# Kernel optimization log

Hardware: AMD Instinct MI355X
Metric: run time of the kernel (lower is better)

## Reference

```python
import jax, jax.numpy as jnp
import numpy as np

N_HEADS = 16
N_KV_HEADS = 4
HEAD_DIM = 128
NEG_INF = -1e9


def setup_inputs() -> dict:
    key = jax.random.key(0)
    ks = jax.random.split(key, 6)
    bs, seq, d_model = 2, 2048, 2048
    x = jax.random.normal(ks[0], (bs, seq, d_model), jnp.float32)
    # RoPE table: theta = 10000^{-2i/head_dim}, angle = pos * theta
    inv_freq = 1.0 / (10000.0 ** (jnp.arange(0, HEAD_DIM, 2, dtype=jnp.float32) / HEAD_DIM))
    ang = jnp.arange(seq, dtype=jnp.float32)[:, None] * inv_freq[None, :]  # [seq, head_dim/2]
    freqs_cos = jnp.cos(ang)
    freqs_sin = jnp.sin(ang)
    # causal additive mask
    mask = jnp.where(jnp.tril(jnp.ones((seq, seq), dtype=bool)), 0.0, NEG_INF).astype(jnp.float32)
    s = 1.0 / np.sqrt(d_model)
    wq = jax.random.normal(ks[1], (d_model, N_HEADS * HEAD_DIM), jnp.float32) * s
    wk = jax.random.normal(ks[2], (d_model, N_KV_HEADS * HEAD_DIM), jnp.float32) * s
    wv = jax.random.normal(ks[3], (d_model, N_KV_HEADS * HEAD_DIM), jnp.float32) * s
    wo = jax.random.normal(ks[4], (N_HEADS * HEAD_DIM, d_model), jnp.float32) * s
    return {"x": x, "freqs_cos": freqs_cos, "freqs_sin": freqs_sin, "mask": mask,
            "wq": wq, "wk": wk, "wv": wv, "wo": wo}


def _rope(t, cos, sin):
    # t: [b, h, s, d]; cos/sin: [s, d/2]
    b, h, s, d = t.shape
    tp = t.reshape(b, h, s, d // 2, 2)
    x0, x1 = tp[..., 0], tp[..., 1]
    c = cos[None, None, :, :]
    sn = sin[None, None, :, :]
    o0 = x0 * c - x1 * sn
    o1 = x0 * sn + x1 * c
    return jnp.stack([o0, o1], axis=-1).reshape(b, h, s, d)


def reference(x, freqs_cos, freqs_sin, mask, wq, wk, wv, wo):
    bs, seq, d_model = x.shape
    rep = N_HEADS // N_KV_HEADS
    q = (x @ wq).reshape(bs, seq, N_HEADS, HEAD_DIM).transpose(0, 2, 1, 3)
    k = (x @ wk).reshape(bs, seq, N_KV_HEADS, HEAD_DIM).transpose(0, 2, 1, 3)
    v = (x @ wv).reshape(bs, seq, N_KV_HEADS, HEAD_DIM).transpose(0, 2, 1, 3)
    q = _rope(q, freqs_cos, freqs_sin)
    k = _rope(k, freqs_cos, freqs_sin)
    # GQA: group q heads over kv heads instead of materially repeating kv
    qg = q.reshape(bs, N_KV_HEADS, rep, seq, HEAD_DIM)
    scores = jnp.einsum('bgrsd,bgtd->bgrst', qg, k) / np.sqrt(HEAD_DIM)
    scores = scores + mask[None, None, None, :, :]
    attn = jax.nn.softmax(scores, axis=-1)
    out = jnp.einsum('bgrst,bgtd->bgrsd', attn, v)
    out = out.reshape(bs, N_HEADS, seq, HEAD_DIM).transpose(0, 2, 1, 3).reshape(bs, seq, -1)
    return out @ wo
```

## Files before the change

kernel.cpp:

```cpp
#include <hip/hip_runtime.h>
#include <hip/hip_bf16.h>

#define SEQ 2048
#define DM 2048
#define NH 16
#define NKV 4
#define HD 128

typedef float f32x4 __attribute__((ext_vector_type(4)));
typedef short s16x8 __attribute__((ext_vector_type(8)));
typedef short s16x4 __attribute__((ext_vector_type(4)));

__device__ inline __hip_bfloat16 f2b(float f) { return __float2bfloat16(f); }
__device__ inline float b2f_us(unsigned short u) { return __uint_as_float(((unsigned)u) << 16); }
__device__ inline short f2b_s(float f) {
    __hip_bfloat16 h = __float2bfloat16(f);
    return *(short*)&h;
}

__device__ inline void gl_lds16(const void* g, void* l) {
    __builtin_amdgcn_global_load_lds((const __attribute__((address_space(1))) void*)g,
                                     (__attribute__((address_space(3))) void*)l, 16, 0, 0);
}

__global__ void prep_kernel(const float* __restrict__ x,
                            const float* __restrict__ wq, const float* __restrict__ wk,
                            const float* __restrict__ wv, const float* __restrict__ wo,
                            __hip_bfloat16* __restrict__ xb,
                            __hip_bfloat16* __restrict__ wqkvt,
                            __hip_bfloat16* __restrict__ wot) {
    __shared__ float tile[32][33];
    int bid = blockIdx.x;
    const int t = threadIdx.x;
    if (bid < 8192) {
        int i = (bid * 256 + t) * 4;
        float4 v = *(const float4*)(x + i);
        __hip_bfloat16 o4[4] = {f2b(v.x), f2b(v.y), f2b(v.z), f2b(v.w)};
        *(ushort4*)(xb + i) = *(ushort4*)o4;
        return;
    }
    bid -= 8192;
    const float* in;
    __hip_bfloat16* out;
    int N, bx, by;
    if (bid < 4096) {
        in = wq; out = wqkvt; N = 2048; bx = bid & 63; by = bid >> 6;
    } else if (bid < 5120) {
        bid -= 4096; in = wk; out = wqkvt + (size_t)2048 * 2048; N = 512; bx = bid & 15; by = bid >> 4;
    } else if (bid < 6144) {
        bid -= 5120; in = wv; out = wqkvt + (size_t)2560 * 2048; N = 512; bx = bid & 15; by = bid >> 4;
    } else {
        bid -= 6144; in = wo; out = wot; N = 2048; bx = bid & 63; by = bid >> 6;
    }
    const int K = 2048;
    int n0 = bx * 32, k0 = by * 32;
    int tx = t & 31, ty = t >> 5;
    for (int r = ty; r < 32; r += 8)
        tile[r][tx] = in[(size_t)(k0 + r) * N + n0 + tx];
    __syncthreads();
    for (int r = ty; r < 32; r += 8)
        out[(size_t)(n0 + r) * K + k0 + tx] = f2b(tile[tx][r]);
}

template <int OUT_F32>
__global__ __launch_bounds__(256, 3) void gemm_bt(
    const __hip_bfloat16* __restrict__ A,
    const __hip_bfloat16* __restrict__ Bt,
    void* __restrict__ Cp, int M, int N, int Kd) {
    __shared__ __hip_bfloat16 As[128 * 64];
    __shared__ __hip_bfloat16 Bs[128 * 64];
    const int nx = gridDim.x, ny = gridDim.y;
    const int pid = blockIdx.y * nx + blockIdx.x;
    const int GM = 8;
    const int grp = pid / (GM * nx);
    const int first = grp * GM;
    const int gsz = (ny - first < GM) ? (ny - first) : GM;
    const int mt = first + (pid % gsz);
    const int ntile = (pid % (GM * nx)) / gsz;
    const int m0 = mt * 128, n0 = ntile * 128;

    const int t = threadIdx.x;
    const int wv = t >> 6, lane = t & 63;
    const int wm = (wv >> 1) * 64, wn = (wv & 1) * 64;
    const int lrow = lane & 15, quad = lane >> 4;
    f32x4 acc[4][4];
    f32x4 z4 = {0.f, 0.f, 0.f, 0.f};
    for (int i = 0; i < 4; ++i)
        for (int j = 0; j < 4; ++j) acc[i][j] = z4;

    for (int k0 = 0; k0 < Kd; k0 += 64) {
        __syncthreads();
        for (int i = 0; i < 4; ++i) {
            int flat = i * 256 + t;
            int row = flat >> 3;
            int cb = (flat & 7) ^ (row & 7);
            gl_lds16(A + (size_t)(m0 + row) * Kd + k0 + cb * 8, &As[flat * 8]);
            gl_lds16(Bt + (size_t)(n0 + row) * Kd + k0 + cb * 8, &Bs[flat * 8]);
        }
        __syncthreads();
        for (int kk = 0; kk < 2; ++kk) {
            s16x8 af[4], bf[4];
            for (int i = 0; i < 4; ++i) {
                int ra = wm + i * 16 + lrow;
                int rb = wn + i * 16 + lrow;
                int pba = ((kk * 4 + quad) ^ (ra & 7)) * 8;
                int pbb = ((kk * 4 + quad) ^ (rb & 7)) * 8;
                af[i] = *(const s16x8*)&As[ra * 64 + pba];
                bf[i] = *(const s16x8*)&Bs[rb * 64 + pbb];
            }
            for (int i = 0; i < 4; ++i)
                for (int j = 0; j < 4; ++j)
                    acc[i][j] = __builtin_amdgcn_mfma_f32_16x16x32_bf16(af[i], bf[j],
                                                                        acc[i][j], 0, 0, 0);
        }
    }
    for (int i = 0; i < 4; ++i)
        for (int j = 0; j < 4; ++j)
            for (int r = 0; r < 4; ++r) {
                int m = m0 + wm + i * 16 + quad * 4 + r;
                int n = n0 + wn + j * 16 + lrow;
                if (OUT_F32)
                    ((float*)Cp)[(size_t)m * N + n] = acc[i][j][r];
                else
                    ((__hip_bfloat16*)Cp)[(size_t)m * N + n] = f2b(acc[i][j][r]);
            }
}

#define QSC 0.12751744f
__global__ void rv_kernel(const __hip_bfloat16* __restrict__ qkv,
                          const float* __restrict__ fcos, const float* __restrict__ fsin,
                          __hip_bfloat16* __restrict__ q, __hip_bfloat16* __restrict__ k,
                          __hip_bfloat16* __restrict__ vt) {
    __shared__ __hip_bfloat16 tile[128][136];
    const int t = threadIdx.x;
    if (blockIdx.x < 4096) {
        int tok = blockIdx.x;
        int b = tok >> 11, s = tok & 2047;
        const __hip_bfloat16* row = qkv + (size_t)tok * 3072;
        for (int it = t; it < 320; it += 256) {
            int col = it * 8;
            s16x8 v = *(const s16x8*)(row + col);
            int p0 = (col & 127) >> 1;
            f32x4 c4 = *(const f32x4*)(fcos + s * 64 + p0);
            f32x4 s4 = *(const f32x4*)(fsin + s * 64 + p0);
            float scl = (col < 2048) ? QSC : 1.0f;
            short outv[8];
            for (int p = 0; p < 4; ++p) {
                float x0 = b2f_us((unsigned short)v[2 * p]);
                float x1 = b2f_us((unsigned short)v[2 * p + 1]);
                outv[2 * p] = f2b_s((x0 * c4[p] - x1 * s4[p]) * scl);
                outv[2 * p + 1] = f2b_s((x0 * s4[p] + x1 * c4[p]) * scl);
            }
            int d = col & 127;
            if (col < 2048) {
                int h = col >> 7;
                *(s16x8*)(q + ((size_t)((b * NH + h) * SEQ + s)) * HD + d) = *(s16x8*)outv;
            } else {
                int h = (col - 2048) >> 7;
                *(s16x8*)(k + ((size_t)((b * NKV + h) * SEQ + s)) * HD + d) = *(s16x8*)outv;
            }
        }
        return;
    }
    int r = blockIdx.x - 4096;
    int s0 = (r & 15) * 128;
    int bh = r >> 4;
    int b = bh >> 2, kvh = bh & 3;
    for (int i = 0; i < 8; ++i) {
        int flat = (i * 256 + t) * 8;
        int row = flat >> 7, col = flat & 127;
        *(s16x8*)&tile[row][col] =
            *(const s16x8*)(qkv + (size_t)(b * SEQ + s0 + row) * 3072 + 2560 + kvh * 128 + col);
    }
    __syncthreads();
    for (int i = 0; i < 8; ++i) {
        int dd = i * 16 + (t >> 4);
        int ss = (t & 15) * 8;
        __hip_bfloat16 tmp[8];
        for (int j = 0; j < 8; ++j) tmp[j] = tile[ss + j][dd];
        *(s16x8*)(vt + ((size_t)((b * NKV + kvh) * HD + dd)) * SEQ + s0 + ss) = *(s16x8*)tmp;
    }
}

__global__ __launch_bounds__(512, 4) void attn_kernel(
    const __hip_bfloat16* __restrict__ q, const __hip_bfloat16* __restrict__ k,
    const __hip_bfloat16* __restrict__ vt, __hip_bfloat16* __restrict__ o) {
    __shared__ __hip_bfloat16 Ks[2][64][136];
    __shared__ __hip_bfloat16 Vs[2][128][72];

    const int bh = blockIdx.y;
    const int bx = (bh < 16) ? (int)(gridDim.x - 1 - blockIdx.x) : (int)blockIdx.x;
    const int b = bh >> 4, h = bh & 15;
    const int kvh = h >> 2;
    const int t = threadIdx.x;
    const int w = t >> 6, lane = t & 63;
    const int lrow = lane & 15, quad = lane >> 4;
    const int q0 = bx * 128;
    const int qrow = q0 + w * 16 + lrow;

    const __hip_bfloat16* qp = q + ((size_t)((b * NH + h) * SEQ + qrow)) * HD;
    s16x8 qf[4];
    for (int ks = 0; ks < 4; ++ks) qf[ks] = *(const s16x8*)(qp + ks * 32 + quad * 8);

    float m_i = -1e30f, l_i = 0.f;
    f32x4 accO[8];
    f32x4 z4 = {0.f, 0.f, 0.f, 0.f};
    for (int d = 0; d < 8; ++d) accO[d] = z4;

    const __hip_bfloat16* kbase = k + ((size_t)(b * NKV + kvh) * SEQ) * HD;
    const __hip_bfloat16* vbase = vt + ((size_t)(b * NKV + kvh) * HD) * SEQ;

    s16x8 kr[2], vr[2];
    auto load_tile = [&](int kt) {
        for (int i = 0; i < 2; ++i) {
            int flat = (i * 512 + t) * 8;
            kr[i] = *(const s16x8*)(kbase + (size_t)(kt * 64 + (flat >> 7)) * HD + (flat & 127));
            vr[i] = *(const s16x8*)(vbase + (size_t)(flat >> 6) * SEQ + kt * 64 + (flat & 63));
        }
    };
    auto store_tile = [&](int bsel) {
        for (int i = 0; i < 2; ++i) {
            int flat = (i * 512 + t) * 8;
            *(s16x8*)&Ks[bsel][flat >> 7][flat & 127] = kr[i];
            int row = flat >> 6, k0 = flat & 63;
            int pb = ((k0 >> 5) << 5) | (((k0 >> 2) & 2) << 3) | (((k0 >> 4) & 1) << 2);
            s16x4 lo = {vr[i][0], vr[i][1], vr[i][2], vr[i][3]};
            s16x4 hi = {vr[i][4], vr[i][5], vr[i][6], vr[i][7]};
            *(s16x4*)&Vs[bsel][row][pb] = lo;
            *(s16x4*)&Vs[bsel][row][pb + 8] = hi;
        }
    };

    const int nkt = 2 * bx + 2;
    load_tile(0);
    store_tile(0);

    for (int kt = 0; kt < nkt; ++kt) {
        const int cur = kt & 1;
        bool more = (kt + 1) < nkt;
        __syncthreads();
        if (more) load_tile(kt + 1);
        bool wave_active = (kt * 64 <= q0 + w * 16 + 15);
        bool mtile = (kt >= 2 * bx);

        if (wave_active) {
            float sv[4][4];
            __builtin_amdgcn_s_setprio(1);
            for (int nt = 0; nt < 4; ++nt) {
                f32x4 sacc = z4;
                for (int ks = 0; ks < 4; ++ks) {
                    s16x8 kf = *(const s16x8*)&Ks[cur][nt * 16 + lrow][ks * 32 + quad * 8];
                    sacc = __builtin_amdgcn_mfma_f32_16x16x32_bf16(kf, qf[ks], sacc, 0, 0, 0);
                }
                if (mtile) {
                    for (int r = 0; r < 4; ++r) {
                        int key = kt * 64 + nt * 16 + quad * 4 + r;
                        sv[nt][r] = (key > qrow) ? -1e30f : sacc[r];
                    }
                } else {
                    for (int r = 0; r < 4; ++r) sv[nt][r] = sacc[r];
                }
            }
            __builtin_amdgcn_s_setprio(0);
            float mt2 = fmaxf(fmaxf(fmaxf(sv[0][0], sv[0][1]), fmaxf(sv[0][2], sv[0][3])),
                              fmaxf(fmaxf(sv[1][0], sv[1][1]), fmaxf(sv[1][2], sv[1][3])));
            mt2 = fmaxf(mt2,
                        fmaxf(fmaxf(fmaxf(sv[2][0], sv[2][1]), fmaxf(sv[2][2], sv[2][3])),
                              fmaxf(fmaxf(sv[3][0], sv[3][1]), fmaxf(sv[3][2], sv[3][3]))));
            mt2 = fmaxf(mt2, __shfl_xor(mt2, 16, 64));
            mt2 = fmaxf(mt2, __shfl_xor(mt2, 32, 64));
            if (!__all(mt2 <= m_i + 8.f)) {
                float mn = fmaxf(m_i, mt2);
                float alpha = exp2f(m_i - mn);
                l_i *= alpha;
                for (int d = 0; d < 8; ++d)
                    for (int r = 0; r < 4; ++r) accO[d][r] *= alpha;
                m_i = mn;
            }
            float rs = 0.f;
            s16x8 pf0, pf1;
#pragma unroll
            for (int j = 0; j < 8; ++j) {
                float p0 = exp2f(sv[j >> 2][j & 3] - m_i);
                float p1 = exp2f(sv[2 + (j >> 2)][j & 3] - m_i);
                rs += p0 + p1;
                pf0[j] = f2b_s(p0);
                pf1[j] = f2b_s(p1);
            }
            rs += __shfl_xor(rs, 16, 64);
            rs += __shfl_xor(rs, 32, 64);
            l_i += rs;
            __builtin_amdgcn_s_setprio(1);
            for (int dt = 0; dt < 8; ++dt) {
                s16x8 vf0 = *(const s16x8*)&Vs[cur][dt * 16 + lrow][quad * 8];
                s16x8 vf1 = *(const s16x8*)&Vs[cur][dt * 16 + lrow][32 + quad * 8];
                accO[dt] = __builtin_amdgcn_mfma_f32_16x16x32_bf16(vf0, pf0, accO[dt], 0, 0, 0);
                accO[dt] = __builtin_amdgcn_mfma_f32_16x16x32_bf16(vf1, pf1, accO[dt], 0, 0, 0);
            }
            __builtin_amdgcn_s_setprio(0);
        }

        if (more) store_tile(1 - cur);
    }
    float inv = 1.0f / l_i;
    __hip_bfloat16* op = o + (size_t)(b * SEQ + qrow) * DM + h * HD;
    for (int dt = 0; dt < 8; ++dt) {
        short ov[4];
        for (int r = 0; r < 4; ++r) ov[r] = f2b_s(accO[dt][r] * inv);
        *(s16x4*)(op + dt * 16 + quad * 4) = *(s16x4*)ov;
    }
}

extern "C" void kernel_launch(void* const* d_in, const int* in_sizes, int n_in,
                              void* d_out, int out_size, void* d_ws, size_t ws_size,
                              hipStream_t stream) {
    (void)in_sizes; (void)n_in; (void)out_size; (void)ws_size;
    const float* x  = (const float*)d_in[0];
    const float* fc = (const float*)d_in[1];
    const float* fs = (const float*)d_in[2];
    const float* wq = (const float*)d_in[4];
    const float* wk = (const float*)d_in[5];
    const float* wv = (const float*)d_in[6];
    const float* wo = (const float*)d_in[7];

    __hip_bfloat16* xb    = (__hip_bfloat16*)d_ws;
    __hip_bfloat16* wqkvt = xb + (size_t)8388608;
    __hip_bfloat16* wot   = wqkvt + (size_t)6291456;
    __hip_bfloat16* qkv   = wot + (size_t)4194304;
    __hip_bfloat16* qb    = xb;
    __hip_bfloat16* kb    = wqkvt;
    __hip_bfloat16* vtb   = wqkvt + (size_t)2097152;
    __hip_bfloat16* attno = qkv;

    prep_kernel<<<18432, 256, 0, stream>>>(x, wq, wk, wv, wo, xb, wqkvt, wot);
    gemm_bt<0><<<dim3(24, 32), 256, 0, stream>>>(xb, wqkvt, qkv, 4096, 3072, 2048);
    rv_kernel<<<4224, 256, 0, stream>>>(qkv, fc, fs, qb, kb, vtb);
    attn_kernel<<<dim3(16, 32), 512, 0, stream>>>(qb, kb, vtb, attno);
    gemm_bt<1><<<dim3(16, 32), 256, 0, stream>>>(attno, wot, d_out, 4096, 2048, 2048);
}
```

Measured before the change: 325.7 us.

## Rewrite GEMM with 256x256 tiles and 4-stage async LDS pipeline

Replaces the 128x128 single-buffered bf16 GEMM with a 256x256-tile, 512-thread kernel. It streams K in steps of 32 through a 4-deep ring of LDS buffers using global_load_lds and explicit vmcnt waits, so loads overlap the MFMA work. It also adds s_setprio around the MFMA block. The larger tiles increase data reuse and cut barrier overhead, at the cost of more LDS (128KB) and more registers per block. The grids shrink to 192 and 128 blocks, which may underfill the 256 CUs.

```diff
diff --git a/kernel.cpp b/kernel.cpp
--- a/kernel.cpp
+++ b/kernel.cpp
@@ -63,12 +63,13 @@
 }
 
 template <int OUT_F32>
-__global__ __launch_bounds__(256, 3) void gemm_bt(
+__global__ __launch_bounds__(512, 2) void gemm256(
     const __hip_bfloat16* __restrict__ A,
     const __hip_bfloat16* __restrict__ Bt,
     void* __restrict__ Cp, int M, int N, int Kd) {
-    __shared__ __hip_bfloat16 As[128 * 64];
-    __shared__ __hip_bfloat16 Bs[128 * 64];
+    __shared__ __hip_bfloat16 As[4][8192];
+    __shared__ __hip_bfloat16 Bs[4][8192];
+
     const int nx = gridDim.x, ny = gridDim.y;
     const int pid = blockIdx.y * nx + blockIdx.x;
     const int GM = 8;
@@ -77,52 +78,82 @@
     const int gsz = (ny - first < GM) ? (ny - first) : GM;
     const int mt = first + (pid % gsz);
     const int ntile = (pid % (GM * nx)) / gsz;
-    const int m0 = mt * 128, n0 = ntile * 128;
+    const int m0 = mt * 256, n0 = ntile * 256;
 
     const int t = threadIdx.x;
-    const int wv = t >> 6, lane = t & 63;
-    const int wm = (wv >> 1) * 64, wn = (wv & 1) * 64;
+    const int wid = t >> 6, lane = t & 63;
+    const int wr = wid >> 2, wc = wid & 3;
     const int lrow = lane & 15, quad = lane >> 4;
-    f32x4 acc[4][4];
+
+    f32x4 acc[8][4];
     f32x4 z4 = {0.f, 0.f, 0.f, 0.f};
-    for (int i = 0; i < 4; ++i)
+#pragma unroll
+    for (int i = 0; i < 8; ++i)
+#pragma unroll
         for (int j = 0; j < 4; ++j) acc[i][j] = z4;
 
-    for (int k0 = 0; k0 < Kd; k0 += 64) {
-        __syncthreads();
-        for (int i = 0; i < 4; ++i) {
-            int flat = i * 256 + t;
-            int row = flat >> 3;
-            int cb = (flat & 7) ^ (row & 7);
-            gl_lds16(A + (size_t)(m0 + row) * Kd + k0 + cb * 8, &As[flat * 8]);
-            gl_lds16(Bt + (size_t)(n0 + row) * Kd + k0 + cb * 8, &Bs[flat * 8]);
-        }
-        __syncthreads();
-        for (int kk = 0; kk < 2; ++kk) {
-            s16x8 af[4], bf[4];
-            for (int i = 0; i < 4; ++i) {
-                int ra = wm + i * 16 + lrow;
-                int rb = wn + i * 16 + lrow;
-                int pba = ((kk * 4 + quad) ^ (ra & 7)) * 8;
-                int pbb = ((kk * 4 + quad) ^ (rb & 7)) * 8;
-                af[i] = *(const s16x8*)&As[ra * 64 + pba];
-                bf[i] = *(const s16x8*)&Bs[rb * 64 + pbb];
-            }
-            for (int i = 0; i < 4; ++i)
-                for (int j = 0; j < 4; ++j)
-                    acc[i][j] = __builtin_amdgcn_mfma_f32_16x16x32_bf16(af[i], bf[j],
-                                                                        acc[i][j], 0, 0, 0);
-        }
-    }
-    for (int i = 0; i < 4; ++i)
-        for (int j = 0; j < 4; ++j)
+    auto stage = [&](int kt) {
+        const int buf = kt & 3;
+#pragma unroll
+        for (int i = 0; i < 2; ++i) {
+            int slot = i * 512 + t;
+            int row = slot >> 2, p = slot & 3;
+            int cb = p ^ ((row >> 1) & 3);
+            gl_lds16(A + (size_t)(m0 + row) * Kd + kt * 32 + cb * 8, &As[buf][slot * 8]);
+            gl_lds16(Bt + (size_t)(n0 + row) * Kd + kt * 32 + cb * 8, &Bs[buf][slot * 8]);
+        }
+    };
+
+    const int nt = Kd >> 5;
+    stage(0); stage(1); stage(2);
+
+    const int psw = quad ^ ((lrow >> 1) & 3);
+
+    for (int kt = 0; kt < nt; ++kt) {
+        if (kt < nt - 2)
+            asm volatile("s_waitcnt vmcnt(8)" ::: "memory");
+        else if (kt == nt - 2)
+            asm volatile("s_waitcnt vmcnt(4)" ::: "memory");
+        else
+            asm volatile("s_waitcnt vmcnt(0)" ::: "memory");
+        __builtin_amdgcn_s_barrier();
+        __builtin_amdgcn_sched_barrier(0);
+        if (kt + 3 < nt) stage(kt + 3);
+
+        const int buf = kt & 3;
+        s16x8 a[8], b[4];
+#pragma unroll
+        for (int mi = 0; mi < 8; ++mi) {
+            int rr = wr * 128 + mi * 16 + lrow;
+            a[mi] = *(const s16x8*)&As[buf][rr * 32 + psw * 8];
+        }
+#pragma unroll
+        for (int ni = 0; ni < 4; ++ni) {
+            int rb = wc * 64 + ni * 16 + lrow;
+            b[ni] = *(const s16x8*)&Bs[buf][rb * 32 + psw * 8];
+        }
+        __builtin_amdgcn_s_setprio(1);
+#pragma unroll
+        for (int mi = 0; mi < 8; ++mi)
+#pragma unroll
+            for (int ni = 0; ni < 4; ++ni)
+                acc[mi][ni] = __builtin_amdgcn_mfma_f32_16x16x32_bf16(a[mi], b[ni],
+                                                                      acc[mi][ni], 0, 0, 0);
+        __builtin_amdgcn_s_setprio(0);
+    }
+
+#pragma unroll
+    for (int mi = 0; mi < 8; ++mi)
+#pragma unroll
+        for (int ni = 0; ni < 4; ++ni)
+#pragma unroll
             for (int r = 0; r < 4; ++r) {
-                int m = m0 + wm + i * 16 + quad * 4 + r;
-                int n = n0 + wn + j * 16 + lrow;
+                int m = m0 + wr * 128 + mi * 16 + quad * 4 + r;
+                int n = n0 + wc * 64 + ni * 16 + lrow;
                 if (OUT_F32)
-                    ((float*)Cp)[(size_t)m * N + n] = acc[i][j][r];
+                    ((float*)Cp)[(size_t)m * N + n] = acc[mi][ni][r];
                 else
-                    ((__hip_bfloat16*)Cp)[(size_t)m * N + n] = f2b(acc[i][j][r]);
+                    ((__hip_bfloat16*)Cp)[(size_t)m * N + n] = f2b(acc[mi][ni][r]);
             }
 }
 
@@ -333,8 +364,8 @@
     __hip_bfloat16* attno = qkv;
 
     prep_kernel<<<18432, 256, 0, stream>>>(x, wq, wk, wv, wo, xb, wqkvt, wot);
-    gemm_bt<0><<<dim3(24, 32), 256, 0, stream>>>(xb, wqkvt, qkv, 4096, 3072, 2048);
+    gemm256<0><<<dim3(12, 16), 512, 0, stream>>>(xb, wqkvt, qkv, 4096, 3072, 2048);
     rv_kernel<<<4224, 256, 0, stream>>>(qkv, fc, fs, qb, kb, vtb);
     attn_kernel<<<dim3(16, 32), 512, 0, stream>>>(qb, kb, vtb, attno);
-    gemm_bt<1><<<dim3(16, 32), 256, 0, stream>>>(attno, wot, d_out, 4096, 2048, 2048);
-}
+    gemm256<1><<<dim3(8, 16), 512, 0, stream>>>(attno, wot, d_out, 4096, 2048, 2048);
+}
```

Result: slower. 383.9 us (+17.8%).
